# Kernel tuning notes

Hardware: AMD Instinct MI355X
Metric: run time of the kernel (lower is better)

The kernel has to match this reference:

```python
import jax, jax.numpy as jnp
import numpy as np

ALPHA = 0.2          # LeakyReLU negative slope
NEG_INF = -9e15      # mask fill value used by the original module


def setup_inputs() -> dict:
    key = jax.random.key(0)
    k1, k2, k3, k4 = jax.random.split(key, 4)
    B, N, Fin, Fout = 8, 2048, 64, 64
    inp = jax.random.normal(k1, (B, N, Fin), dtype=jnp.float32)
    adj = jax.random.randint(k2, (N, N), 0, 2, dtype=jnp.int32)
    # kaiming-normal-ish scale for W, xavier-normal-ish for a
    W = jax.random.normal(k3, (Fin, Fout), dtype=jnp.float32) * np.sqrt(2.0 / Fout)
    a = jax.random.normal(k4, (2 * Fout, 1), dtype=jnp.float32) * np.sqrt(2.0 / (2 * Fout + 1))
    return {"input": inp, "adj": adj, "W": W, "a": a}


def reference(input, adj, W, a):
    # h: [B, N, Fout]
    h = jnp.matmul(input, W)
    Fout = W.shape[1]
    a1 = a[:Fout, 0]   # weights for source node h_i
    a2 = a[Fout:, 0]   # weights for target node h_j
    # e[b,i,j] = leaky_relu(h_i . a1 + h_j . a2) -- equivalent to the
    # original cat([h_i, h_j]) @ a without materializing [B,N,N,2F].
    s1 = jnp.einsum('bnf,f->bn', h, a1)  # [B, N]
    s2 = jnp.einsum('bnf,f->bn', h, a2)  # [B, N]
    e = s1[:, :, None] + s2[:, None, :]  # [B, N, N]
    e = jnp.where(e > 0, e, ALPHA * e)   # LeakyReLU
    # mask by adjacency (broadcast [N,N] over batch), stable softmax over j
    masked = jnp.where(adj[None, :, :] > 0, e, NEG_INF)
    attention = jax.nn.softmax(masked, axis=-1)  # dropout=0.0 (eval)
    h_prime = jnp.matmul(attention, h)           # [B, N, Fout]
    return jax.nn.elu(h_prime)                   # concat=True branch
```

## Files before the change

kernel.cpp:

```cpp
#include <hip/hip_runtime.h>


typedef __attribute__((ext_vector_type(8))) short s16x8;
typedef __attribute__((ext_vector_type(8))) unsigned short u16x8;
typedef __attribute__((ext_vector_type(4))) float f32x4;

#define ALPHA 0.2f
#define NEGINF -9000000000000000.0f

__device__ __forceinline__ unsigned short f2bf(float f) {
  unsigned int x = __float_as_uint(f);
  x += 0x7fffu + ((x >> 16) & 1u);
  return (unsigned short)(x >> 16);
}
__device__ __forceinline__ float bf2f(unsigned short h) {
  return __uint_as_float(((unsigned int)h) << 16);
}

__global__ __launch_bounds__(256) void gat_prep(
    const float* __restrict__ inp, const float* __restrict__ W,
    const float* __restrict__ a,
    unsigned short* __restrict__ hT_hi, unsigned short* __restrict__ hT_lo,
    float* __restrict__ s1, float* __restrict__ s2)
{
  const int b  = blockIdx.y;
  const int n0 = blockIdx.x * 64;
  const int t  = threadIdx.x;

  __shared__ float Wl[64 * 64];
  __shared__ float il[64 * 64];
  __shared__ float ht[64 * 65];

  for (int idx = t; idx < 4096; idx += 256) Wl[idx] = W[idx];
  const float* ib = inp + ((size_t)b * 2048 + n0) * 64;
  for (int idx = t; idx < 4096; idx += 256) il[idx] = ib[idx];
  __syncthreads();

  const int w = t >> 6, lane = t & 63;
  float wreg[64];
  #pragma unroll
  for (int k = 0; k < 64; ++k) wreg[k] = Wl[k * 64 + lane];
  const float a1 = a[lane], a2 = a[64 + lane];

  for (int r8 = 0; r8 < 16; ++r8) {
    const int row = w * 16 + r8;
    float acc = 0.f;
    #pragma unroll
    for (int k4 = 0; k4 < 16; ++k4) {
      float4 iv = *(const float4*)&il[row * 64 + k4 * 4];
      acc += iv.x * wreg[k4 * 4 + 0];
      acc += iv.y * wreg[k4 * 4 + 1];
      acc += iv.z * wreg[k4 * 4 + 2];
      acc += iv.w * wreg[k4 * 4 + 3];
    }
    ht[row * 65 + lane] = acc;
    float p1 = acc * a1, p2 = acc * a2;
    #pragma unroll
    for (int off = 32; off; off >>= 1) {
      p1 += __shfl_xor(p1, off);
      p2 += __shfl_xor(p2, off);
    }
    if (lane == 0) {
      s1[b * 2048 + n0 + row] = p1;
      s2[b * 2048 + n0 + row] = p2;
    }
  }
  __syncthreads();

  const int f = t >> 2, nl = (t & 3) * 16;
  u16x8 hi0, hi1, lo0, lo1;
  #pragma unroll
  for (int q = 0; q < 16; ++q) {
    float v = ht[(nl + q) * 65 + f];
    unsigned short hb = f2bf(v);
    float lov = v - bf2f(hb);
    unsigned short lb = f2bf(lov);
    if (q < 8) { hi0[q] = hb; lo0[q] = lb; }
    else       { hi1[q - 8] = hb; lo1[q - 8] = lb; }
  }
  size_t base = ((size_t)b * 64 + f) * 2048 + n0 + nl;
  *(u16x8*)(hT_hi + base)     = hi0;
  *(u16x8*)(hT_hi + base + 8) = hi1;
  *(u16x8*)(hT_lo + base)     = lo0;
  *(u16x8*)(hT_lo + base + 8) = lo1;
}

__global__ __launch_bounds__(256) void gat_attn(
    const int* __restrict__ adj,
    const unsigned short* __restrict__ hT_hi, const unsigned short* __restrict__ hT_lo,
    const float* __restrict__ s1, const float* __restrict__ s2,
    float* __restrict__ out)
{
  const int b  = blockIdx.y;
  const int i0 = blockIdx.x * 64;
  const int t  = threadIdx.x;
  const int w  = t >> 6, l = t & 63;
  const int r  = l & 15, g = l >> 4;

  __shared__ float s2l[2048];
  __shared__ unsigned short hhi[64 * 40];
  __shared__ unsigned short hlo[64 * 40];

  for (int idx = t * 4; idx < 2048; idx += 1024)
    *(float4*)&s2l[idx] = *(const float4*)&s2[b * 2048 + idx];

  const int irow = i0 + w * 16 + r;
  const float s1r = s1[b * 2048 + irow];
  const int* adjp = adj + (size_t)irow * 2048 + g * 8;
  const unsigned short* ghi = hT_hi + (size_t)b * 64 * 2048;
  const unsigned short* glo = hT_lo + (size_t)b * 64 * 2048;

  float m = NEGINF, lsum = 0.f;
  f32x4 acc[4];
  #pragma unroll
  for (int c = 0; c < 4; ++c) acc[c] = (f32x4){0.f, 0.f, 0.f, 0.f};

  const int sf = t >> 2, sj = (t & 3) * 8;

  for (int j0 = 0; j0 < 2048; j0 += 32) {
    __syncthreads();
    *(u16x8*)&hhi[sf * 40 + sj] = *(const u16x8*)(ghi + sf * 2048 + j0 + sj);
    *(u16x8*)&hlo[sf * 40 + sj] = *(const u16x8*)(glo + sf * 2048 + j0 + sj);
    __syncthreads();

    int4 ad0 = *(const int4*)(adjp + j0);
    int4 ad1 = *(const int4*)(adjp + j0 + 4);
    float4 sv0 = *(const float4*)&s2l[j0 + g * 8];
    float4 sv1 = *(const float4*)&s2l[j0 + g * 8 + 4];
    float e[8];
    e[0] = s1r + sv0.x; e[1] = s1r + sv0.y; e[2] = s1r + sv0.z; e[3] = s1r + sv0.w;
    e[4] = s1r + sv1.x; e[5] = s1r + sv1.y; e[6] = s1r + sv1.z; e[7] = s1r + sv1.w;
    const int adv[8] = {ad0.x, ad0.y, ad0.z, ad0.w, ad1.x, ad1.y, ad1.z, ad1.w};
    #pragma unroll
    for (int k = 0; k < 8; ++k) {
      float le = fmaxf(e[k], ALPHA * e[k]);
      e[k] = adv[k] > 0 ? le : NEGINF;
    }

    float tm = e[0];
    #pragma unroll
    for (int k = 1; k < 8; ++k) tm = fmaxf(tm, e[k]);
    tm = fmaxf(tm, __shfl_xor(tm, 16));
    tm = fmaxf(tm, __shfl_xor(tm, 32));
    const float mnew  = fmaxf(m, tm);
    const float scale = __expf(m - mnew);
    float p[8], ts = 0.f;
    #pragma unroll
    for (int k = 0; k < 8; ++k) { p[k] = __expf(e[k] - mnew); ts += p[k]; }
    ts += __shfl_xor(ts, 16);
    ts += __shfl_xor(ts, 32);
    lsum = lsum * scale + ts;
    m = mnew;

    float sc[4];
    #pragma unroll
    for (int q = 0; q < 4; ++q) sc[q] = __shfl(scale, g * 4 + q);
    #pragma unroll
    for (int c = 0; c < 4; ++c) {
      #pragma unroll
      for (int q = 0; q < 4; ++q) acc[c][q] *= sc[q];
    }

    s16x8 phi, plo;
    #pragma unroll
    for (int k = 0; k < 8; ++k) {
      unsigned short hb = f2bf(p[k]);
      phi[k] = (short)hb;
      plo[k] = (short)f2bf(p[k] - bf2f(hb));
    }

    #pragma unroll
    for (int c = 0; c < 4; ++c) {
      s16x8 bh = *(const s16x8*)&hhi[(c * 16 + r) * 40 + g * 8];
      s16x8 bl = *(const s16x8*)&hlo[(c * 16 + r) * 40 + g * 8];
      acc[c] = __builtin_amdgcn_mfma_f32_16x16x32_bf16(phi, bh, acc[c], 0, 0, 0);
      acc[c] = __builtin_amdgcn_mfma_f32_16x16x32_bf16(phi, bl, acc[c], 0, 0, 0);
      acc[c] = __builtin_amdgcn_mfma_f32_16x16x32_bf16(plo, bh, acc[c], 0, 0, 0);
    }
  }

  float inv[4];
  #pragma unroll
  for (int q = 0; q < 4; ++q) inv[q] = 1.f / __shfl(lsum, g * 4 + q);
  #pragma unroll
  for (int c = 0; c < 4; ++c) {
    #pragma unroll
    for (int q = 0; q < 4; ++q) {
      float v = acc[c][q] * inv[q];
      v = v > 0.f ? v : __expf(v) - 1.f;
      out[((size_t)b * 2048 + i0 + w * 16 + g * 4 + q) * 64 + c * 16 + r] = v;
    }
  }
}

extern "C" void kernel_launch(void* const* d_in, const int* in_sizes, int n_in,
                              void* d_out, int out_size, void* d_ws, size_t ws_size,
                              hipStream_t stream) {
  (void)in_sizes; (void)n_in; (void)out_size; (void)ws_size;
  const float* inp = (const float*)d_in[0];
  const int*   adj = (const int*)d_in[1];
  const float* W   = (const float*)d_in[2];
  const float* a   = (const float*)d_in[3];
  float* out = (float*)d_out;

  char* ws = (char*)d_ws;
  unsigned short* hT_hi = (unsigned short*)ws;
  unsigned short* hT_lo = (unsigned short*)(ws + (2u << 20));
  float* s1 = (float*)(ws + (4u << 20));
  float* s2 = (float*)(ws + (4u << 20) + (64u << 10));

  dim3 grid(32, 8);
  gat_prep<<<grid, 256, 0, stream>>>(inp, W, a, hT_hi, hT_lo, s1, s2);
  gat_attn<<<grid, 256, 0, stream>>>(adj, hT_hi, hT_lo, s1, s2, out);
}
```

Before: 166.8 us.

## Split attention key dimension across waves with LDS merge of partial softmax

Each block now handles 16 query rows instead of 64, and its four waves each process a quarter of the 2048 keys. Partial max, sum and accumulators are merged through shared memory at the end. The h tiles are read straight from global memory instead of staged in LDS, which removes per-iteration barriers, and the adjacency loads are prefetched one iteration ahead. The grid grows fourfold to 1024 blocks for better occupancy, at the cost of more global/L2 traffic for h and an extra reduction step.

```diff
diff --git a/kernel.cpp b/kernel.cpp
--- a/kernel.cpp
+++ b/kernel.cpp
@@ -92,19 +92,20 @@
     float* __restrict__ out)
 {
   const int b  = blockIdx.y;
-  const int i0 = blockIdx.x * 64;
+  const int i0 = blockIdx.x * 16;
   const int t  = threadIdx.x;
   const int w  = t >> 6, l = t & 63;
   const int r  = l & 15, g = l >> 4;
 
   __shared__ float s2l[2048];
-  __shared__ unsigned short hhi[64 * 40];
-  __shared__ unsigned short hlo[64 * 40];
+  __shared__ float accbuf[4][16][64];
+  __shared__ float mlbuf[4][16][2];
 
   for (int idx = t * 4; idx < 2048; idx += 1024)
     *(float4*)&s2l[idx] = *(const float4*)&s2[b * 2048 + idx];
-
-  const int irow = i0 + w * 16 + r;
+  __syncthreads();
+
+  const int irow = i0 + r;
   const float s1r = s1[b * 2048 + irow];
   const int* adjp = adj + (size_t)irow * 2048 + g * 8;
   const unsigned short* ghi = hT_hi + (size_t)b * 64 * 2048;
@@ -115,16 +116,16 @@
   #pragma unroll
   for (int c = 0; c < 4; ++c) acc[c] = (f32x4){0.f, 0.f, 0.f, 0.f};
 
-  const int sf = t >> 2, sj = (t & 3) * 8;
-
-  for (int j0 = 0; j0 < 2048; j0 += 32) {
-    __syncthreads();
-    *(u16x8*)&hhi[sf * 40 + sj] = *(const u16x8*)(ghi + sf * 2048 + j0 + sj);
-    *(u16x8*)&hlo[sf * 40 + sj] = *(const u16x8*)(glo + sf * 2048 + j0 + sj);
-    __syncthreads();
-
-    int4 ad0 = *(const int4*)(adjp + j0);
-    int4 ad1 = *(const int4*)(adjp + j0 + 4);
+  const int jw0 = w * 512;
+  int4 ad0 = *(const int4*)(adjp + jw0);
+  int4 ad1 = *(const int4*)(adjp + jw0 + 4);
+
+  for (int it = 0; it < 16; ++it) {
+    const int j0 = jw0 + it * 32;
+    const int jn = (it < 15) ? j0 + 32 : j0;
+    int4 nad0 = *(const int4*)(adjp + jn);
+    int4 nad1 = *(const int4*)(adjp + jn + 4);
+
     float4 sv0 = *(const float4*)&s2l[j0 + g * 8];
     float4 sv1 = *(const float4*)&s2l[j0 + g * 8 + 4];
     float e[8];
@@ -171,26 +172,46 @@
 
     #pragma unroll
     for (int c = 0; c < 4; ++c) {
-      s16x8 bh = *(const s16x8*)&hhi[(c * 16 + r) * 40 + g * 8];
-      s16x8 bl = *(const s16x8*)&hlo[(c * 16 + r) * 40 + g * 8];
+      const size_t fo = (size_t)(c * 16 + r) * 2048 + j0 + g * 8;
+      s16x8 bh = *(const s16x8*)(ghi + fo);
+      s16x8 bl = *(const s16x8*)(glo + fo);
       acc[c] = __builtin_amdgcn_mfma_f32_16x16x32_bf16(phi, bh, acc[c], 0, 0, 0);
       acc[c] = __builtin_amdgcn_mfma_f32_16x16x32_bf16(phi, bl, acc[c], 0, 0, 0);
       acc[c] = __builtin_amdgcn_mfma_f32_16x16x32_bf16(plo, bh, acc[c], 0, 0, 0);
     }
-  }
-
-  float inv[4];
-  #pragma unroll
-  for (int q = 0; q < 4; ++q) inv[q] = 1.f / __shfl(lsum, g * 4 + q);
+
+    ad0 = nad0; ad1 = nad1;
+  }
+
+  if (l < 16) { mlbuf[w][r][0] = m; mlbuf[w][r][1] = lsum; }
   #pragma unroll
   for (int c = 0; c < 4; ++c) {
     #pragma unroll
-    for (int q = 0; q < 4; ++q) {
-      float v = acc[c][q] * inv[q];
-      v = v > 0.f ? v : __expf(v) - 1.f;
-      out[((size_t)b * 2048 + i0 + w * 16 + g * 4 + q) * 64 + c * 16 + r] = v;
-    }
-  }
+    for (int q = 0; q < 4; ++q) accbuf[w][g * 4 + q][c * 16 + r] = acc[c][q];
+  }
+  __syncthreads();
+
+  const int row = t >> 4, fb = (t & 15) * 4;
+  float mw[4], lw[4];
+  #pragma unroll
+  for (int v = 0; v < 4; ++v) { mw[v] = mlbuf[v][row][0]; lw[v] = mlbuf[v][row][1]; }
+  float M = fmaxf(fmaxf(mw[0], mw[1]), fmaxf(mw[2], mw[3]));
+  float L = 0.f, wx[4];
+  #pragma unroll
+  for (int v = 0; v < 4; ++v) { wx[v] = __expf(mw[v] - M); L += lw[v] * wx[v]; }
+  float4 o = {0.f, 0.f, 0.f, 0.f};
+  #pragma unroll
+  for (int v = 0; v < 4; ++v) {
+    float4 av = *(const float4*)&accbuf[v][row][fb];
+    o.x += av.x * wx[v]; o.y += av.y * wx[v];
+    o.z += av.z * wx[v]; o.w += av.w * wx[v];
+  }
+  const float invL = 1.f / L;
+  float ov[4] = {o.x * invL, o.y * invL, o.z * invL, o.w * invL};
+  #pragma unroll
+  for (int k = 0; k < 4; ++k) ov[k] = ov[k] > 0.f ? ov[k] : __expf(ov[k]) - 1.f;
+  float4 res = {ov[0], ov[1], ov[2], ov[3]};
+  *(float4*)&out[((size_t)b * 2048 + i0 + row) * 64 + fb] = res;
 }
 
 extern "C" void kernel_launch(void* const* d_in, const int* in_sizes, int n_in,
@@ -209,7 +230,6 @@
   float* s1 = (float*)(ws + (4u << 20));
   float* s2 = (float*)(ws + (4u << 20) + (64u << 10));
 
-  dim3 grid(32, 8);
-  gat_prep<<<grid, 256, 0, stream>>>(inp, W, a, hT_hi, hT_lo, s1, s2);
-  gat_attn<<<grid, 256, 0, stream>>>(adj, hT_hi, hT_lo, s1, s2, out);
-}
+  gat_prep<<<dim3(32, 8), 256, 0, stream>>>(inp, W, a, hT_hi, hT_lo, s1, s2);
+  gat_attn<<<dim3(128, 8), 256, 0, stream>>>(adj, hT_hi, hT_lo, s1, s2, out);
+}
```

Measured after the change: 156.1 us. 6.4% less time.
